# Kernel optimization log

Hardware: AMD Instinct MI355X
Metric: run time of the kernel (lower is better)

The kernel has to match this reference:

```python
import jax, jax.numpy as jnp
import numpy as np

H = 1152
NH = 16
HD = H // NH
CTX = 768
MLP = int(H * 4.0)
EPS = 1e-6


def _ln(x):
    mu = jnp.mean(x, axis=-1, keepdims=True)
    var = jnp.mean(jnp.square(x - mu), axis=-1, keepdims=True)
    return (x - mu) / jnp.sqrt(var + EPS)


def _modulate(x, shift, scale):
    return x * (1 + scale[:, None, :]) + shift[:, None, :]


def _gelu_tanh(x):
    c = jnp.float32(np.sqrt(2.0 / np.pi))
    return 0.5 * x * (1.0 + jnp.tanh(c * (x + 0.044715 * x * x * x)))


def _heads(t, nh):
    B, N, C = t.shape
    return t.reshape(B, N, nh, C // nh).transpose(0, 2, 1, 3)  # [B,h,N,hd]


def setup_inputs() -> dict:
    key = jax.random.key(0)
    ks = jax.random.split(key, 20)
    s = lambda fan_in: 1.0 / np.sqrt(fan_in)
    d = {
        'x': jax.random.normal(ks[0], (8, 1024, H), jnp.float32),
        'c': jax.random.normal(ks[1], (8, 77, CTX), jnp.float32),
        't_emb': jax.random.normal(ks[2], (8, H), jnp.float32),
        'qkv_w': jax.random.normal(ks[3], (3 * H, H), jnp.float32) * s(H),
        'qkv_b': jnp.zeros((3 * H,), jnp.float32),
        'proj_w': jax.random.normal(ks[4], (H, H), jnp.float32) * s(H),
        'proj_b': jnp.zeros((H,), jnp.float32),
        'to_q_w': jax.random.normal(ks[5], (H, H), jnp.float32) * s(H),
        'to_k_w': jax.random.normal(ks[6], (H, CTX), jnp.float32) * s(CTX),
        'to_v_w': jax.random.normal(ks[7], (H, CTX), jnp.float32) * s(CTX),
        'to_out_w': jax.random.normal(ks[8], (H, H), jnp.float32) * s(H),
        'to_out_b': jnp.zeros((H,), jnp.float32),
        'mlp_w1': jax.random.normal(ks[9], (MLP, H), jnp.float32) * s(H),
        'mlp_b1': jnp.zeros((MLP,), jnp.float32),
        'mlp_w2': jax.random.normal(ks[10], (H, MLP), jnp.float32) * s(MLP),
        'mlp_b2': jnp.zeros((H,), jnp.float32),
        'ada_w': jax.random.normal(ks[11], (6 * H, H), jnp.float32) * s(H),
        'ada_b': jnp.zeros((6 * H,), jnp.float32),
    }
    return d


def reference(x, c, t_emb, qkv_w, qkv_b, proj_w, proj_b, to_q_w, to_k_w, to_v_w,
              to_out_w, to_out_b, mlp_w1, mlp_b1, mlp_w2, mlp_b2, ada_w, ada_b):
    B, N, C = x.shape
    scale = HD ** -0.5

    # adaLN modulation
    mod = jax.nn.silu(t_emb) @ ada_w.T + ada_b  # [B,6H]
    sh_msa, sc_msa, g_msa, sh_mlp, sc_mlp, g_mlp = jnp.split(mod, 6, axis=1)

    # self-attention
    h = _modulate(_ln(x), sh_msa, sc_msa)
    qkv = h @ qkv_w.T + qkv_b  # [B,N,3H]
    q, k, v = jnp.split(qkv, 3, axis=-1)
    q, k, v = _heads(q, NH), _heads(k, NH), _heads(v, NH)
    attn = jax.nn.softmax(jnp.einsum('bhnd,bhmd->bhnm', q, k) * scale, axis=-1)
    o = jnp.einsum('bhnm,bhmd->bhnd', attn, v).transpose(0, 2, 1, 3).reshape(B, N, C)
    x = x + g_msa[:, None, :] * (o @ proj_w.T + proj_b)

    # cross-attention
    q = _heads(x @ to_q_w.T, NH)
    k = _heads(c @ to_k_w.T, NH)
    v = _heads(c @ to_v_w.T, NH)
    attn = jax.nn.softmax(jnp.einsum('bhnd,bhmd->bhnm', q, k) * scale, axis=-1)
    o = jnp.einsum('bhnm,bhmd->bhnd', attn, v).transpose(0, 2, 1, 3).reshape(B, N, C)
    x = x + (o @ to_out_w.T + to_out_b)

    # gated MLP
    h = _modulate(_ln(x), sh_mlp, sc_mlp)
    h = _gelu_tanh(h @ mlp_w1.T + mlp_b1) @ mlp_w2.T + mlp_b2
    return x + g_mlp[:, None, :] * h
```

## Files before the change

### kernel.cpp

```cpp
#include <hip/hip_runtime.h>
#include <stdint.h>

typedef __bf16 bf16;
typedef bf16 bf16x8 __attribute__((ext_vector_type(8)));
typedef bf16 bf16x4 __attribute__((ext_vector_type(4)));
typedef float f32x4 __attribute__((ext_vector_type(4)));

#define DEV __device__ __forceinline__


DEV void gload_lds16(const bf16* g, bf16* l) {
  __builtin_amdgcn_global_load_lds((const __attribute__((address_space(1))) void*)g,
                                   (__attribute__((address_space(3))) void*)l,
                                   16, 0, 0);
}

DEV uint32_t pkbf(float a, float b) {
  unsigned short ua = __builtin_bit_cast(unsigned short, (bf16)a);
  unsigned short ub = __builtin_bit_cast(unsigned short, (bf16)b);
  return (uint32_t)ua | ((uint32_t)ub << 16);
}

union U8 { uint32_t u[4]; bf16x8 v; };


__global__ void f2b_kernel(const float* __restrict__ in, bf16* __restrict__ out, int n4) {
  int i = blockIdx.x * 256 + threadIdx.x;
  if (i < n4) {
    float4 v = ((const float4*)in)[i];
    bf16x4 o;
    o[0] = (bf16)v.x; o[1] = (bf16)v.y; o[2] = (bf16)v.z; o[3] = (bf16)v.w;
    *(bf16x4*)(out + (size_t)i * 4) = o;
  }
}


__global__ void silu_kernel(const float* __restrict__ in, float* __restrict__ out, int n) {
  int i = blockIdx.x * 256 + threadIdx.x;
  if (i < n) { float v = in[i]; out[i] = v / (1.0f + __expf(-v)); }
}


__global__ __launch_bounds__(256) void mod_kernel(
    const float* __restrict__ st, const float* __restrict__ ada_w,
    const float* __restrict__ ada_b, float* __restrict__ modout) {
  int gw = (blockIdx.x * 256 + threadIdx.x) >> 6;
  int lane = threadIdx.x & 63;
  if (gw >= 8 * 6912) return;
  int b = gw / 6912, j = gw % 6912;
  const float* sp = st + b * 1152;
  const float* wp = ada_w + (size_t)j * 1152;
  float acc = 0.f;
  for (int k = lane; k < 1152; k += 64) acc += sp[k] * wp[k];
  #pragma unroll
  for (int off = 32; off; off >>= 1) acc += __shfl_xor(acc, off);
  if (lane == 0) modout[(size_t)b * 6912 + j] = acc + ada_b[j];
}


__global__ __launch_bounds__(256) void ln_mod_kernel(
    const float* __restrict__ x, const float* __restrict__ mod,
    int sh_off, int sc_off, bf16* __restrict__ out) {
  int row = blockIdx.x, tid = threadIdx.x;
  int b = row >> 10;
  const float* xr = x + (size_t)row * 1152;
  float vals[5];
  float s = 0.f, s2 = 0.f;
  #pragma unroll
  for (int it = 0; it < 5; ++it) {
    int i = tid + it * 256;
    float v = (i < 1152) ? xr[i] : 0.f;
    vals[it] = v; s += v; s2 += v * v;
  }
  #pragma unroll
  for (int off = 32; off; off >>= 1) { s += __shfl_xor(s, off); s2 += __shfl_xor(s2, off); }
  __shared__ float rs[4], rs2[4];
  int w = tid >> 6, lane = tid & 63;
  if (lane == 0) { rs[w] = s; rs2[w] = s2; }
  __syncthreads();
  s = rs[0] + rs[1] + rs[2] + rs[3];
  s2 = rs2[0] + rs2[1] + rs2[2] + rs2[3];
  float mu = s * (1.0f / 1152.0f);
  float var = s2 * (1.0f / 1152.0f) - mu * mu;
  float rstd = rsqrtf(var + 1e-6f);
  const float* shp = mod + (size_t)b * 6912 + sh_off;
  const float* scp = mod + (size_t)b * 6912 + sc_off;
  #pragma unroll
  for (int it = 0; it < 5; ++it) {
    int i = tid + it * 256;
    if (i < 1152) {
      float v = (vals[it] - mu) * rstd;
      out[(size_t)row * 1152 + i] = (bf16)(v * (1.0f + scp[i]) + shp[i]);
    }
  }
}


DEV void stage_tile(const bf16* src, int ld, int row0, int maxrow, int k0,
                    bf16* lds, int tid) {
  int lane = tid & 63, wv = tid >> 6;
  #pragma unroll
  for (int j = 0; j < 2; ++j) {
    int r = j * 64 + wv * 16 + (lane >> 2);
    int kk = (lane & 3) * 8;
    int gr = min(row0 + r, maxrow);
    const bf16* g = src + (size_t)gr * ld + k0 + kk;
    bf16* l = lds + (j * 64 + wv * 16) * 32;
    gload_lds16(g, l);
  }
}

template <int EP>
__global__ __launch_bounds__(256) void gemm_bt(
    const bf16* __restrict__ A, int lda,
    const bf16* __restrict__ W, int ldw,
    const float* __restrict__ bias,
    bf16* __restrict__ Cb, int ldc,
    float* __restrict__ Cf,
    const float* __restrict__ resid,
    const float* __restrict__ gate, int gate_off,
    bf16* __restrict__ Cb2,
    int M, int N, int K) {
  __shared__ __align__(16) bf16 lA[128 * 32];
  __shared__ __align__(16) bf16 lB[128 * 32];
  int tid = threadIdx.x, lane = tid & 63, w = tid >> 6;
  int wr = w >> 1, wc = w & 1;
  int row0 = blockIdx.x * 128, col0 = blockIdx.y * 128;
  f32x4 acc[4][4] = {};
  int nk = K >> 5;
  int rbase = wr * 64 + (lane & 15);
  int cbase = wc * 64 + (lane & 15);
  int koff = (lane >> 4) * 8;
  for (int ks = 0; ks < nk; ++ks) {
    stage_tile(A, lda, row0, M - 1, ks * 32, lA, tid);
    stage_tile(W, ldw, col0, N - 1, ks * 32, lB, tid);
    __syncthreads();
    bf16x8 af[4], bg[4];
    #pragma unroll
    for (int i = 0; i < 4; ++i) af[i] = *(const bf16x8*)&lA[(rbase + i * 16) * 32 + koff];
    #pragma unroll
    for (int i = 0; i < 4; ++i) bg[i] = *(const bf16x8*)&lB[(cbase + i * 16) * 32 + koff];
    #pragma unroll
    for (int mi = 0; mi < 4; ++mi)
      #pragma unroll
      for (int ni = 0; ni < 4; ++ni)
        acc[mi][ni] = __builtin_amdgcn_mfma_f32_16x16x32_bf16(af[mi], bg[ni], acc[mi][ni], 0, 0, 0);
    __syncthreads();
  }
  int r0 = row0 + wr * 64, c0 = col0 + wc * 64;
  #pragma unroll
  for (int mi = 0; mi < 4; ++mi)
    #pragma unroll
    for (int ni = 0; ni < 4; ++ni)
      #pragma unroll
      for (int rg = 0; rg < 4; ++rg) {
        int r = r0 + mi * 16 + (lane >> 4) * 4 + rg;
        int cc = c0 + ni * 16 + (lane & 15);
        if (r < M) {
          float v = acc[mi][ni][rg];
          if (bias) v += bias[cc];
          if constexpr (EP == 0) {
            Cb[(size_t)r * ldc + cc] = (bf16)v;
          } else if constexpr (EP == 1) {
            float gt = gate ? gate[(size_t)(r >> 10) * 6912 + gate_off + cc] : 1.0f;
            float o = resid[(size_t)r * ldc + cc] + gt * v;
            Cf[(size_t)r * ldc + cc] = o;
            if (Cb2) Cb2[(size_t)r * ldc + cc] = (bf16)o;
          } else {
            float t = tanhf(0.7978845608028654f * (v + 0.044715f * v * v * v));
            Cb[(size_t)r * ldc + cc] = (bf16)(0.5f * v * (1.0f + t));
          }
        }
      }
}


__global__ __launch_bounds__(256) void attn_kernel(
    const bf16* __restrict__ Q, long q_b, int q_h_off, int q_ld,
    const bf16* __restrict__ K, long k_b, int k_h_off, int k_ld,
    const bf16* __restrict__ V, long v_b, int v_h_off, int v_ld,
    bf16* __restrict__ O, long o_b, int o_h_off, int o_ld,
    int Nk, float scale) {
  __shared__ __align__(16) bf16 lK[32 * 104];
  __shared__ __align__(16) bf16 lVT[80 * 40];
  int tid = threadIdx.x, lane = tid & 63, w = tid >> 6;
  int bz = blockIdx.z, hy = blockIdx.y;
  int q0 = blockIdx.x * 64;
  int g = lane >> 4, i16 = lane & 15;
  const bf16* Qb = Q + (long)bz * q_b + hy * q_h_off;
  const bf16* Kb = K + (long)bz * k_b + hy * k_h_off;
  const bf16* Vb = V + (long)bz * v_b + hy * v_h_off;
  int qr = q0 + w * 16 + i16;
  const bf16* qrow = Qb + (long)qr * q_ld;
  bf16x8 qf[3];
  qf[0] = *(const bf16x8*)(qrow + g * 8);
  qf[1] = *(const bf16x8*)(qrow + 32 + g * 8);
  if (g == 0) qf[2] = *(const bf16x8*)(qrow + 64);
  else { bf16x8 z = {}; qf[2] = z; }
  float m = -1e30f, l = 0.f;
  f32x4 ot[5] = {};
  for (int k0 = 0; k0 < Nk; k0 += 32) {
    __syncthreads();
    for (int idx = tid; idx < 32 * 48; idx += 256) {
      int r = idx / 48, d = (idx % 48) * 2;
      int krow = k0 + r;
      uint32_t val = 0;
      if (krow < Nk && d < 72) val = *(const uint32_t*)(Kb + (long)krow * k_ld + d);
      *(uint32_t*)&lK[r * 104 + d] = val;
    }
    for (int idx = tid; idx < 32 * 40; idx += 256) {
      int r = idx / 40, d = (idx % 40) * 2;
      int vrow = k0 + r;
      uint32_t val = 0;
      if (vrow < Nk && d < 72) val = *(const uint32_t*)(Vb + (long)vrow * v_ld + d);
      lVT[d * 40 + r]       = __builtin_bit_cast(bf16, (unsigned short)(val & 0xffffu));
      lVT[(d + 1) * 40 + r] = __builtin_bit_cast(bf16, (unsigned short)(val >> 16));
    }
    __syncthreads();
    f32x4 sa = {}, sb = {};
    #pragma unroll
    for (int cD = 0; cD < 3; ++cD) {
      bf16x8 ka = *(const bf16x8*)&lK[i16 * 104 + cD * 32 + g * 8];
      bf16x8 kb = *(const bf16x8*)&lK[(16 + i16) * 104 + cD * 32 + g * 8];
      sa = __builtin_amdgcn_mfma_f32_16x16x32_bf16(ka, qf[cD], sa, 0, 0, 0);
      sb = __builtin_amdgcn_mfma_f32_16x16x32_bf16(kb, qf[cD], sb, 0, 0, 0);
    }
    float p[8];
    #pragma unroll
    for (int r = 0; r < 4; ++r) { p[r] = sa[r] * scale; p[4 + r] = sb[r] * scale; }
    if (k0 + 32 > Nk) {
      #pragma unroll
      for (int r = 0; r < 4; ++r) {
        if (k0 + g * 4 + r >= Nk)      p[r]     = -1e30f;
        if (k0 + 16 + g * 4 + r >= Nk) p[4 + r] = -1e30f;
      }
    }
    float tm = p[0];
    #pragma unroll
    for (int j = 1; j < 8; ++j) tm = fmaxf(tm, p[j]);
    tm = fmaxf(tm, __shfl_xor(tm, 16));
    tm = fmaxf(tm, __shfl_xor(tm, 32));
    float mnew = fmaxf(m, tm);
    float alpha = __expf(m - mnew);
    float psum = 0.f;
    #pragma unroll
    for (int j = 0; j < 8; ++j) { p[j] = __expf(p[j] - mnew); psum += p[j]; }
    psum += __shfl_xor(psum, 16);
    psum += __shfl_xor(psum, 32);
    l = l * alpha + psum;
    m = mnew;
    #pragma unroll
    for (int dt = 0; dt < 5; ++dt) ot[dt] *= alpha;
    uint32_t dA0 = pkbf(p[0], p[1]), dA1 = pkbf(p[2], p[3]);
    uint32_t dB0 = pkbf(p[4], p[5]), dB1 = pkbf(p[6], p[7]);
    int s0 = ((2 * g) & 3) * 16 + i16;
    int s1 = s0 + 16;
    uint32_t wa0 = (uint32_t)__shfl((int)dA0, s0), wa1 = (uint32_t)__shfl((int)dA1, s0);
    uint32_t wa2 = (uint32_t)__shfl((int)dA0, s1), wa3 = (uint32_t)__shfl((int)dA1, s1);
    uint32_t wb0 = (uint32_t)__shfl((int)dB0, s0), wb1 = (uint32_t)__shfl((int)dB1, s0);
    uint32_t wb2 = (uint32_t)__shfl((int)dB0, s1), wb3 = (uint32_t)__shfl((int)dB1, s1);
    U8 pu;
    pu.u[0] = g < 2 ? wa0 : wb0;
    pu.u[1] = g < 2 ? wa1 : wb1;
    pu.u[2] = g < 2 ? wa2 : wb2;
    pu.u[3] = g < 2 ? wa3 : wb3;
    #pragma unroll
    for (int dt = 0; dt < 5; ++dt) {
      bf16x8 vt = *(const bf16x8*)&lVT[(dt * 16 + i16) * 40 + g * 8];
      ot[dt] = __builtin_amdgcn_mfma_f32_16x16x32_bf16(vt, pu.v, ot[dt], 0, 0, 0);
    }
  }
  float inv = 1.0f / l;
  bf16* orow = O + (long)bz * o_b + (long)hy * o_h_off + (long)(q0 + w * 16 + i16) * o_ld;
  #pragma unroll
  for (int dt = 0; dt < 5; ++dt)
    #pragma unroll
    for (int rg = 0; rg < 4; ++rg) {
      int d = dt * 16 + g * 4 + rg;
      if (d < 72) orow[d] = (bf16)(ot[dt][rg] * inv);
    }
}


extern "C" void kernel_launch(void* const* d_in, const int* in_sizes, int n_in,
                              void* d_out, int out_size, void* d_ws, size_t ws_size,
                              hipStream_t stream) {
  (void)in_sizes; (void)n_in; (void)out_size; (void)ws_size;
  const float* x        = (const float*)d_in[0];
  const float* c        = (const float*)d_in[1];
  const float* t_emb    = (const float*)d_in[2];
  const float* qkv_w    = (const float*)d_in[3];
  const float* qkv_b    = (const float*)d_in[4];
  const float* proj_w   = (const float*)d_in[5];
  const float* proj_b   = (const float*)d_in[6];
  const float* to_q_w   = (const float*)d_in[7];
  const float* to_k_w   = (const float*)d_in[8];
  const float* to_v_w   = (const float*)d_in[9];
  const float* to_out_w = (const float*)d_in[10];
  const float* to_out_b = (const float*)d_in[11];
  const float* mlp_w1   = (const float*)d_in[12];
  const float* mlp_b1   = (const float*)d_in[13];
  const float* mlp_w2   = (const float*)d_in[14];
  const float* mlp_b2   = (const float*)d_in[15];
  const float* ada_w    = (const float*)d_in[16];
  const float* ada_b    = (const float*)d_in[17];
  float* out = (float*)d_out;

  char* ws = (char*)d_ws;
  size_t off = 0;
  auto alloc = [&](size_t b) { size_t o = off; off += (b + 255) & ~(size_t)255; return o; };
  bf16* wq    = (bf16*)(ws + alloc((size_t)3456 * 1152 * 2));
  bf16* wproj = (bf16*)(ws + alloc((size_t)1152 * 1152 * 2));
  bf16* wtoq  = (bf16*)(ws + alloc((size_t)1152 * 1152 * 2));
  bf16* wtok  = (bf16*)(ws + alloc((size_t)1152 * 768 * 2));
  bf16* wtov  = (bf16*)(ws + alloc((size_t)1152 * 768 * 2));
  bf16* wtoout= (bf16*)(ws + alloc((size_t)1152 * 1152 * 2));
  bf16* wm1   = (bf16*)(ws + alloc((size_t)4608 * 1152 * 2));
  bf16* wm2   = (bf16*)(ws + alloc((size_t)1152 * 4608 * 2));
  bf16* cb    = (bf16*)(ws + alloc((size_t)616 * 768 * 2));
  float* stl  = (float*)(ws + alloc((size_t)8 * 1152 * 4));
  float* modb = (float*)(ws + alloc((size_t)8 * 6912 * 4));
  bf16* S1    = (bf16*)(ws + alloc((size_t)8192 * 1152 * 2));
  bf16* R1    = (bf16*)(ws + alloc((size_t)8192 * 4608 * 2));
  bf16* R2    = (bf16*)(ws + alloc((size_t)8192 * 1152 * 2));
  float* x2   = (float*)(ws + alloc((size_t)8192 * 1152 * 4));

  bf16* qkvbuf = R1;
  bf16* q2 = R1;
  bf16* kc = (bf16*)((char*)R1 + (size_t)8192 * 1152 * 2);
  bf16* vc = (bf16*)((char*)kc + (size_t)616 * 1152 * 2);
  bf16* mid = R1;

  auto cvt = [&](const float* src, bf16* dst, size_t n) {
    int n4 = (int)(n / 4);
    f2b_kernel<<<(n4 + 255) / 256, 256, 0, stream>>>(src, dst, n4);
  };
  cvt(qkv_w,    wq,    (size_t)3456 * 1152);
  cvt(proj_w,   wproj, (size_t)1152 * 1152);
  cvt(to_q_w,   wtoq,  (size_t)1152 * 1152);
  cvt(to_k_w,   wtok,  (size_t)1152 * 768);
  cvt(to_v_w,   wtov,  (size_t)1152 * 768);
  cvt(to_out_w, wtoout,(size_t)1152 * 1152);
  cvt(mlp_w1,   wm1,   (size_t)4608 * 1152);
  cvt(mlp_w2,   wm2,   (size_t)1152 * 4608);
  cvt(c,        cb,    (size_t)616 * 768);

  silu_kernel<<<36, 256, 0, stream>>>(t_emb, stl, 8 * 1152);
  mod_kernel<<<13824, 256, 0, stream>>>(stl, ada_w, ada_b, modb);

  ln_mod_kernel<<<8192, 256, 0, stream>>>(x, modb, 0, 1152, S1);

  gemm_bt<0><<<dim3(64, 27), 256, 0, stream>>>(S1, 1152, wq, 1152, qkv_b,
      qkvbuf, 3456, nullptr, nullptr, nullptr, 0, nullptr, 8192, 3456, 1152);

  const float scale = 0.11785113019775793f;
  attn_kernel<<<dim3(16, 16, 8), 256, 0, stream>>>(
      qkvbuf,        (long)1024 * 3456, 72, 3456,
      qkvbuf + 1152, (long)1024 * 3456, 72, 3456,
      qkvbuf + 2304, (long)1024 * 3456, 72, 3456,
      R2,            (long)1024 * 1152, 72, 1152,
      1024, scale);

  gemm_bt<1><<<dim3(64, 9), 256, 0, stream>>>(R2, 1152, wproj, 1152, proj_b,
      nullptr, 1152, x2, x, modb, 2304, S1, 8192, 1152, 1152);

  gemm_bt<0><<<dim3(64, 9), 256, 0, stream>>>(S1, 1152, wtoq, 1152, nullptr,
      q2, 1152, nullptr, nullptr, nullptr, 0, nullptr, 8192, 1152, 1152);
  gemm_bt<0><<<dim3(5, 9), 256, 0, stream>>>(cb, 768, wtok, 768, nullptr,
      kc, 1152, nullptr, nullptr, nullptr, 0, nullptr, 616, 1152, 768);
  gemm_bt<0><<<dim3(5, 9), 256, 0, stream>>>(cb, 768, wtov, 768, nullptr,
      vc, 1152, nullptr, nullptr, nullptr, 0, nullptr, 616, 1152, 768);

  attn_kernel<<<dim3(16, 16, 8), 256, 0, stream>>>(
      q2, (long)1024 * 1152, 72, 1152,
      kc, (long)77 * 1152,   72, 1152,
      vc, (long)77 * 1152,   72, 1152,
      R2, (long)1024 * 1152, 72, 1152,
      77, scale);

  gemm_bt<1><<<dim3(64, 9), 256, 0, stream>>>(R2, 1152, wtoout, 1152, to_out_b,
      nullptr, 1152, out, x2, nullptr, 0, nullptr, 8192, 1152, 1152);

  ln_mod_kernel<<<8192, 256, 0, stream>>>(out, modb, 3456, 4608, S1);

  gemm_bt<2><<<dim3(64, 36), 256, 0, stream>>>(S1, 1152, wm1, 1152, mlp_b1,
      mid, 4608, nullptr, nullptr, nullptr, 0, nullptr, 8192, 4608, 1152);

  gemm_bt<1><<<dim3(64, 9), 256, 0, stream>>>(mid, 4608, wm2, 4608, mlp_b2,
      nullptr, 1152, out, out, modb, 5760, nullptr, 8192, 1152, 4608);
}
```

Baseline: 1.373 ms.

## Process four query tiles per wave in attention to reuse K/V tiles

Each wave now handles 64 query rows (four 16-row groups) instead of 16, so every staged K and V tile in LDS is reused four times and the grid shrinks from 16 to 4 blocks along the query axis. The K/V loads are also vectorised to 16-byte global loads, and the K padding columns are zeroed once up front. The cost is many more live registers (accumulators and Q fragments), which may lower occupancy, and fewer blocks in flight (512 total).

```diff
diff --git a/kernel.cpp b/kernel.cpp
--- a/kernel.cpp
+++ b/kernel.cpp
@@ -185,100 +185,141 @@
   __shared__ __align__(16) bf16 lVT[80 * 40];
   int tid = threadIdx.x, lane = tid & 63, w = tid >> 6;
   int bz = blockIdx.z, hy = blockIdx.y;
-  int q0 = blockIdx.x * 64;
+  int q0 = blockIdx.x * 256;
   int g = lane >> 4, i16 = lane & 15;
-  const bf16* Qb = Q + (long)bz * q_b + hy * q_h_off;
-  const bf16* Kb = K + (long)bz * k_b + hy * k_h_off;
-  const bf16* Vb = V + (long)bz * v_b + hy * v_h_off;
-  int qr = q0 + w * 16 + i16;
-  const bf16* qrow = Qb + (long)qr * q_ld;
-  bf16x8 qf[3];
-  qf[0] = *(const bf16x8*)(qrow + g * 8);
-  qf[1] = *(const bf16x8*)(qrow + 32 + g * 8);
-  if (g == 0) qf[2] = *(const bf16x8*)(qrow + 64);
-  else { bf16x8 z = {}; qf[2] = z; }
-  float m = -1e30f, l = 0.f;
-  f32x4 ot[5] = {};
+  const bf16* Qb = Q + (long)bz * q_b + (long)hy * q_h_off;
+  const bf16* Kb = K + (long)bz * k_b + (long)hy * k_h_off;
+  const bf16* Vb = V + (long)bz * v_b + (long)hy * v_h_off;
+
+  bf16x8 qf[4][3];
+  #pragma unroll
+  for (int qp = 0; qp < 4; ++qp) {
+    const bf16* qrow = Qb + (long)(q0 + w * 64 + qp * 16 + i16) * q_ld;
+    qf[qp][0] = *(const bf16x8*)(qrow + g * 8);
+    qf[qp][1] = *(const bf16x8*)(qrow + 32 + g * 8);
+    if (g == 0) qf[qp][2] = *(const bf16x8*)(qrow + 64);
+    else { bf16x8 z = {}; qf[qp][2] = z; }
+  }
+
+  for (int i = tid; i < 512; i += 256) {
+    int r = i >> 4, cu = i & 15;
+    ((uint32_t*)lK)[r * 52 + 36 + cu] = 0;
+  }
+
+  float m[4], l[4];
+  #pragma unroll
+  for (int qp = 0; qp < 4; ++qp) { m[qp] = -1e30f; l[qp] = 0.f; }
+  f32x4 ot[5][4] = {};
+
   for (int k0 = 0; k0 < Nk; k0 += 32) {
     __syncthreads();
-    for (int idx = tid; idx < 32 * 48; idx += 256) {
-      int r = idx / 48, d = (idx % 48) * 2;
-      int krow = k0 + r;
-      uint32_t val = 0;
-      if (krow < Nk && d < 72) val = *(const uint32_t*)(Kb + (long)krow * k_ld + d);
-      *(uint32_t*)&lK[r * 104 + d] = val;
-    }
-    for (int idx = tid; idx < 32 * 40; idx += 256) {
-      int r = idx / 40, d = (idx % 40) * 2;
-      int vrow = k0 + r;
-      uint32_t val = 0;
-      if (vrow < Nk && d < 72) val = *(const uint32_t*)(Vb + (long)vrow * v_ld + d);
-      lVT[d * 40 + r]       = __builtin_bit_cast(bf16, (unsigned short)(val & 0xffffu));
-      lVT[(d + 1) * 40 + r] = __builtin_bit_cast(bf16, (unsigned short)(val >> 16));
+    #pragma unroll
+    for (int s = 0; s < 2; ++s) {
+      int cidx = tid + s * 256;
+      if (cidx < 288) {
+        int r = cidx & 31, cch = cidx >> 5;
+        int krow = k0 + r;
+        uint4 val = {0, 0, 0, 0};
+        if (krow < Nk) val = *(const uint4*)(Kb + (long)krow * k_ld + cch * 8);
+        *(uint4*)&lK[r * 104 + cch * 8] = val;
+      }
+    }
+    #pragma unroll
+    for (int s = 0; s < 2; ++s) {
+      int cidx = tid + s * 256;
+      if (cidx < 288) {
+        int r = cidx & 31, cch = cidx >> 5;
+        int vrow = k0 + r;
+        uint4 val = {0, 0, 0, 0};
+        if (vrow < Nk) val = *(const uint4*)(Vb + (long)vrow * v_ld + cch * 8);
+        uint32_t uu[4] = {val.x, val.y, val.z, val.w};
+        #pragma unroll
+        for (int j = 0; j < 4; ++j) {
+          lVT[(cch * 8 + 2 * j) * 40 + r]     = __builtin_bit_cast(bf16, (unsigned short)(uu[j] & 0xffffu));
+          lVT[(cch * 8 + 2 * j + 1) * 40 + r] = __builtin_bit_cast(bf16, (unsigned short)(uu[j] >> 16));
+        }
+      }
     }
     __syncthreads();
-    f32x4 sa = {}, sb = {};
+
+    bf16x8 ka[3], kb[3];
     #pragma unroll
     for (int cD = 0; cD < 3; ++cD) {
-      bf16x8 ka = *(const bf16x8*)&lK[i16 * 104 + cD * 32 + g * 8];
-      bf16x8 kb = *(const bf16x8*)&lK[(16 + i16) * 104 + cD * 32 + g * 8];
-      sa = __builtin_amdgcn_mfma_f32_16x16x32_bf16(ka, qf[cD], sa, 0, 0, 0);
-      sb = __builtin_amdgcn_mfma_f32_16x16x32_bf16(kb, qf[cD], sb, 0, 0, 0);
-    }
-    float p[8];
-    #pragma unroll
-    for (int r = 0; r < 4; ++r) { p[r] = sa[r] * scale; p[4 + r] = sb[r] * scale; }
-    if (k0 + 32 > Nk) {
-      #pragma unroll
-      for (int r = 0; r < 4; ++r) {
-        if (k0 + g * 4 + r >= Nk)      p[r]     = -1e30f;
-        if (k0 + 16 + g * 4 + r >= Nk) p[4 + r] = -1e30f;
-      }
-    }
-    float tm = p[0];
-    #pragma unroll
-    for (int j = 1; j < 8; ++j) tm = fmaxf(tm, p[j]);
-    tm = fmaxf(tm, __shfl_xor(tm, 16));
-    tm = fmaxf(tm, __shfl_xor(tm, 32));
-    float mnew = fmaxf(m, tm);
-    float alpha = __expf(m - mnew);
-    float psum = 0.f;
-    #pragma unroll
-    for (int j = 0; j < 8; ++j) { p[j] = __expf(p[j] - mnew); psum += p[j]; }
-    psum += __shfl_xor(psum, 16);
-    psum += __shfl_xor(psum, 32);
-    l = l * alpha + psum;
-    m = mnew;
-    #pragma unroll
-    for (int dt = 0; dt < 5; ++dt) ot[dt] *= alpha;
-    uint32_t dA0 = pkbf(p[0], p[1]), dA1 = pkbf(p[2], p[3]);
-    uint32_t dB0 = pkbf(p[4], p[5]), dB1 = pkbf(p[6], p[7]);
-    int s0 = ((2 * g) & 3) * 16 + i16;
-    int s1 = s0 + 16;
-    uint32_t wa0 = (uint32_t)__shfl((int)dA0, s0), wa1 = (uint32_t)__shfl((int)dA1, s0);
-    uint32_t wa2 = (uint32_t)__shfl((int)dA0, s1), wa3 = (uint32_t)__shfl((int)dA1, s1);
-    uint32_t wb0 = (uint32_t)__shfl((int)dB0, s0), wb1 = (uint32_t)__shfl((int)dB1, s0);
-    uint32_t wb2 = (uint32_t)__shfl((int)dB0, s1), wb3 = (uint32_t)__shfl((int)dB1, s1);
-    U8 pu;
-    pu.u[0] = g < 2 ? wa0 : wb0;
-    pu.u[1] = g < 2 ? wa1 : wb1;
-    pu.u[2] = g < 2 ? wa2 : wb2;
-    pu.u[3] = g < 2 ? wa3 : wb3;
+      ka[cD] = *(const bf16x8*)&lK[i16 * 104 + cD * 32 + g * 8];
+      kb[cD] = *(const bf16x8*)&lK[(16 + i16) * 104 + cD * 32 + g * 8];
+    }
+
+    bf16x8 pu[4];
+    #pragma unroll
+    for (int qp = 0; qp < 4; ++qp) {
+      f32x4 sa = {}, sb = {};
+      #pragma unroll
+      for (int cD = 0; cD < 3; ++cD) {
+        sa = __builtin_amdgcn_mfma_f32_16x16x32_bf16(ka[cD], qf[qp][cD], sa, 0, 0, 0);
+        sb = __builtin_amdgcn_mfma_f32_16x16x32_bf16(kb[cD], qf[qp][cD], sb, 0, 0, 0);
+      }
+      float p[8];
+      #pragma unroll
+      for (int r = 0; r < 4; ++r) { p[r] = sa[r] * scale; p[4 + r] = sb[r] * scale; }
+      if (k0 + 32 > Nk) {
+        #pragma unroll
+        for (int r = 0; r < 4; ++r) {
+          if (k0 + g * 4 + r >= Nk)      p[r]     = -1e30f;
+          if (k0 + 16 + g * 4 + r >= Nk) p[4 + r] = -1e30f;
+        }
+      }
+      float tm = p[0];
+      #pragma unroll
+      for (int j = 1; j < 8; ++j) tm = fmaxf(tm, p[j]);
+      tm = fmaxf(tm, __shfl_xor(tm, 16));
+      tm = fmaxf(tm, __shfl_xor(tm, 32));
+      float mnew = fmaxf(m[qp], tm);
+      float alpha = __expf(m[qp] - mnew);
+      float psum = 0.f;
+      #pragma unroll
+      for (int j = 0; j < 8; ++j) { p[j] = __expf(p[j] - mnew); psum += p[j]; }
+      psum += __shfl_xor(psum, 16);
+      psum += __shfl_xor(psum, 32);
+      l[qp] = l[qp] * alpha + psum;
+      m[qp] = mnew;
+      #pragma unroll
+      for (int dt = 0; dt < 5; ++dt) ot[dt][qp] *= alpha;
+      uint32_t dA0 = pkbf(p[0], p[1]), dA1 = pkbf(p[2], p[3]);
+      uint32_t dB0 = pkbf(p[4], p[5]), dB1 = pkbf(p[6], p[7]);
+      int s0 = ((2 * g) & 3) * 16 + i16;
+      int s1 = s0 + 16;
+      uint32_t wa0 = (uint32_t)__shfl((int)dA0, s0), wa1 = (uint32_t)__shfl((int)dA1, s0);
+      uint32_t wa2 = (uint32_t)__shfl((int)dA0, s1), wa3 = (uint32_t)__shfl((int)dA1, s1);
+      uint32_t wb0 = (uint32_t)__shfl((int)dB0, s0), wb1 = (uint32_t)__shfl((int)dB1, s0);
+      uint32_t wb2 = (uint32_t)__shfl((int)dB0, s1), wb3 = (uint32_t)__shfl((int)dB1, s1);
+      U8 puu;
+      puu.u[0] = g < 2 ? wa0 : wb0;
+      puu.u[1] = g < 2 ? wa1 : wb1;
+      puu.u[2] = g < 2 ? wa2 : wb2;
+      puu.u[3] = g < 2 ? wa3 : wb3;
+      pu[qp] = puu.v;
+    }
     #pragma unroll
     for (int dt = 0; dt < 5; ++dt) {
       bf16x8 vt = *(const bf16x8*)&lVT[(dt * 16 + i16) * 40 + g * 8];
-      ot[dt] = __builtin_amdgcn_mfma_f32_16x16x32_bf16(vt, pu.v, ot[dt], 0, 0, 0);
-    }
-  }
-  float inv = 1.0f / l;
-  bf16* orow = O + (long)bz * o_b + (long)hy * o_h_off + (long)(q0 + w * 16 + i16) * o_ld;
-  #pragma unroll
-  for (int dt = 0; dt < 5; ++dt)
-    #pragma unroll
-    for (int rg = 0; rg < 4; ++rg) {
-      int d = dt * 16 + g * 4 + rg;
-      if (d < 72) orow[d] = (bf16)(ot[dt][rg] * inv);
-    }
+      #pragma unroll
+      for (int qp = 0; qp < 4; ++qp)
+        ot[dt][qp] = __builtin_amdgcn_mfma_f32_16x16x32_bf16(vt, pu[qp], ot[dt][qp], 0, 0, 0);
+    }
+  }
+  #pragma unroll
+  for (int qp = 0; qp < 4; ++qp) {
+    float inv = 1.0f / l[qp];
+    bf16* orow = O + (long)bz * o_b + (long)hy * o_h_off +
+                 (long)(q0 + w * 64 + qp * 16 + i16) * o_ld;
+    #pragma unroll
+    for (int dt = 0; dt < 5; ++dt)
+      #pragma unroll
+      for (int rg = 0; rg < 4; ++rg) {
+        int d = dt * 16 + g * 4 + rg;
+        if (d < 72) orow[d] = (bf16)(ot[dt][qp][rg] * inv);
+      }
+  }
 }
 
 
@@ -354,7 +395,7 @@
       qkvbuf, 3456, nullptr, nullptr, nullptr, 0, nullptr, 8192, 3456, 1152);
 
   const float scale = 0.11785113019775793f;
-  attn_kernel<<<dim3(16, 16, 8), 256, 0, stream>>>(
+  attn_kernel<<<dim3(4, 16, 8), 256, 0, stream>>>(
       qkvbuf,        (long)1024 * 3456, 72, 3456,
       qkvbuf + 1152, (long)1024 * 3456, 72, 3456,
       qkvbuf + 2304, (long)1024 * 3456, 72, 3456,
@@ -371,7 +412,7 @@
   gemm_bt<0><<<dim3(5, 9), 256, 0, stream>>>(cb, 768, wtov, 768, nullptr,
       vc, 1152, nullptr, nullptr, nullptr, 0, nullptr, 616, 1152, 768);
 
-  attn_kernel<<<dim3(16, 16, 8), 256, 0, stream>>>(
+  attn_kernel<<<dim3(4, 16, 8), 256, 0, stream>>>(
       q2, (long)1024 * 1152, 72, 1152,
       kc, (long)77 * 1152,   72, 1152,
       vc, (long)77 * 1152,   72, 1152,
```

Result: faster. 1.260 ms (-8.2%).
